# Optimization experiments

Hardware: AMD Instinct MI355X
Metric: run time of the kernel (lower is better)

The kernel has to match this reference:

```python
import jax, jax.numpy as jnp
import numpy as np

D_HEAD = 64
EPS_NORM = 1e-6
EPS_COS = 1e-6


def rms_norm(x, scale, eps=EPS_NORM):
    mean_sq = jnp.mean(x * x, axis=-1, keepdims=True)
    return x * (scale * jax.lax.rsqrt(mean_sq + eps))


def setup_inputs() -> dict:
    key = jax.random.key(0)
    ks = jax.random.split(key, 8)
    b, l, d, d_ff = 2, 2048, 1024, 3072
    std = 1.0 / np.sqrt(d)
    return {
        "x": jax.random.normal(ks[0], (b, l, d), jnp.float32),
        "pos": jax.random.normal(ks[1], (b, l, 2), jnp.float32),
        "norm_scale": jnp.ones((d,), jnp.float32),
        "w_qkv": jax.random.normal(ks[2], (3 * d, d), jnp.float32) * std,
        "attn_scale": jnp.full((d // D_HEAD,), 10.0, jnp.float32),
        "w_out": jax.random.normal(ks[3], (d, d), jnp.float32) * std,
        "ff_norm_scale": jnp.ones((d,), jnp.float32),
        "w_up": jax.random.normal(ks[4], (2 * d_ff, d), jnp.float32) * std,
        "w_down": jax.random.normal(ks[5], (d, d_ff), jnp.float32) * (1.0 / np.sqrt(d_ff)),
    }


def reference(x, pos, norm_scale, w_qkv, attn_scale, w_out, ff_norm_scale, w_up, w_down):
    n, l, d = x.shape
    nh = d // D_HEAD

    # ---- self-attention block ----
    skip = x
    xn = rms_norm(x, norm_scale)
    qkv = xn @ w_qkv.T                                    # [n, l, 3d]
    qkv = qkv.reshape(n, l, 3, nh, D_HEAD).transpose(2, 0, 3, 1, 4)  # [3, n, nh, l, e]
    q, k, v = qkv[0], qkv[1], qkv[2]

    # cosine-similarity rescaling with per-head learned scale
    s = attn_scale[:, None, None]                         # [nh, 1, 1]
    sqrt_s = jnp.sqrt(s)
    q = q * (sqrt_s * jax.lax.rsqrt(jnp.sum(q * q, axis=-1, keepdims=True) + EPS_COS))
    k = k * (sqrt_s * jax.lax.rsqrt(jnp.sum(k * k, axis=-1, keepdims=True) + EPS_COS))

    # SDPA with scale=1.0 (no RoPE: rope_cls=None)
    scores = jnp.einsum("nhqe,nhke->nhqk", q, k)
    attn = jax.nn.softmax(scores, axis=-1)
    o = jnp.einsum("nhqk,nhke->nhqe", attn, v)            # [n, nh, l, e]
    o = o.transpose(0, 2, 1, 3).reshape(n, l, d)
    x = o @ w_out.T + skip

    # ---- feed-forward block (SwiGLU) ----
    skip = x
    xn = rms_norm(x, ff_norm_scale)
    u = xn @ w_up.T                                       # [n, l, 2*d_ff]
    a, g = jnp.split(u, 2, axis=-1)
    h = a * jax.nn.silu(g)
    x = h @ w_down.T + skip
    return x
```

## Files before the change

kernel.cpp:

```cpp
#include <hip/hip_runtime.h>
#include <cstdint>
#include <cstddef>
#include <cstdio>


typedef unsigned short u16;
typedef __bf16 bf16x8 __attribute__((ext_vector_type(8)));
typedef float  f32x4  __attribute__((ext_vector_type(4)));

__device__ __forceinline__ u16 f2b(float f) {
  return __builtin_bit_cast(u16, (__bf16)f);
}
__device__ __forceinline__ float b2f(u16 u) {
  return (float)__builtin_bit_cast(__bf16, u);
}

__device__ __forceinline__ void cp16(const u16* g, u16* l) {
  __builtin_amdgcn_global_load_lds(
      (__attribute__((address_space(1))) void*)(uintptr_t)g,
      (__attribute__((address_space(3))) void*)(uintptr_t)l,
      16, 0, 0);
}

template <int MODE>
__global__ __launch_bounds__(256) void gemm_bt(
    const u16* __restrict__ A, const u16* __restrict__ B,
    float* __restrict__ Cf, u16* __restrict__ Cb, const float* __restrict__ res,
    int M, int N, int K, int lda)
{
  __shared__ __align__(16) u16 lsA[128 * 64];
  __shared__ __align__(16) u16 lsB[128 * 64];
  const int t = threadIdx.x;
  const int w = t >> 6, lane = t & 63;
  const int wm = (w >> 1) * 64, wn = (w & 1) * 64;
  const int lr = lane & 15, quad = lane >> 4;
  const int cswz = lr & 7;
  const size_t rowA0 = (size_t)blockIdx.x * 128;
  const size_t rowB0 = (size_t)blockIdx.y * 128;

  f32x4 acc[4][4] = {};

  for (int k0 = 0; k0 < K; k0 += 64) {
#pragma unroll
    for (int i = 0; i < 4; ++i) {
      const int id = i * 256 + t;
      const int r = id >> 3;
      const int c = ((id & 7) ^ (r & 7)) * 8;
      cp16(A + (rowA0 + r) * lda + k0 + c, lsA + id * 8);
      cp16(B + (rowB0 + r) * (size_t)K + k0 + c, lsB + id * 8);
    }
    __syncthreads();
#pragma unroll
    for (int ks = 0; ks < 2; ++ks) {
      const int co = ((ks * 4 + quad) ^ cswz) * 8;
      bf16x8 af[4], bfr[4];
#pragma unroll
      for (int i = 0; i < 4; ++i) {
        af[i]  = *(const bf16x8*)(lsA + (wm + i * 16 + lr) * 64 + co);
        bfr[i] = *(const bf16x8*)(lsB + (wn + i * 16 + lr) * 64 + co);
      }
#pragma unroll
      for (int mi = 0; mi < 4; ++mi)
#pragma unroll
        for (int ni = 0; ni < 4; ++ni)
          acc[mi][ni] = __builtin_amdgcn_mfma_f32_16x16x32_bf16(
              af[mi], bfr[ni], acc[mi][ni], 0, 0, 0);
    }
    __syncthreads();
  }

#pragma unroll
  for (int mi = 0; mi < 4; ++mi) {
#pragma unroll
    for (int r = 0; r < 4; ++r) {
      const size_t m = rowA0 + wm + mi * 16 + quad * 4 + r;
#pragma unroll
      for (int ni = 0; ni < 4; ++ni) {
        const size_t n = rowB0 + wn + ni * 16 + lr;
        const size_t o = m * (size_t)N + n;
        const float v = acc[mi][ni][r];
        if (MODE == 0) Cf[o] = v;
        else if (MODE == 1) Cf[o] = v + res[o];
        else Cb[o] = f2b(v);
      }
    }
  }
}

__global__ __launch_bounds__(256) void rmsnorm_k(
    const float* __restrict__ x, const float* __restrict__ g, u16* __restrict__ out)
{
  const int row = blockIdx.x;
  const int t = threadIdx.x;
  const float4 a = ((const float4*)(x + (size_t)row * 1024))[t];
  float ss = a.x * a.x + a.y * a.y + a.z * a.z + a.w * a.w;
#pragma unroll
  for (int o = 32; o; o >>= 1) ss += __shfl_xor(ss, o, 64);
  __shared__ float red[4];
  if ((t & 63) == 0) red[t >> 6] = ss;
  __syncthreads();
  ss = red[0] + red[1] + red[2] + red[3];
  const float r = rsqrtf(ss * (1.0f / 1024.0f) + 1e-6f);
  const float4 gg = ((const float4*)g)[t];
  ushort4 o4;
  o4.x = f2b(a.x * gg.x * r);
  o4.y = f2b(a.y * gg.y * r);
  o4.z = f2b(a.z * gg.z * r);
  o4.w = f2b(a.w * gg.w * r);
  ((ushort4*)out)[(size_t)row * 256 + t] = o4;
}

__global__ __launch_bounds__(256) void cvt_bf16_k(
    const float* __restrict__ in, u16* __restrict__ out)
{
  const size_t i = (size_t)blockIdx.x * 256 + threadIdx.x;
  const float4 v = ((const float4*)in)[i];
  ushort4 o4;
  o4.x = f2b(v.x); o4.y = f2b(v.y); o4.z = f2b(v.z); o4.w = f2b(v.w);
  ((ushort4*)out)[i] = o4;
}

__global__ __launch_bounds__(256) void qkv_prep_k(
    const u16* __restrict__ qkv, const float* __restrict__ attn_scale,
    u16* __restrict__ Qb, u16* __restrict__ Kb, u16* __restrict__ Vt)
{
  const int l0 = blockIdx.x * 64;
  const int h  = blockIdx.y;
  const int nb = blockIdx.z;
  const int t = threadIdx.x, w = t >> 6, lane = t & 63;
  __shared__ float lsV[64][65];
  const float sq = sqrtf(attn_scale[h]);
  const int head = nb * 16 + h;
#pragma unroll 4
  for (int i = 0; i < 16; ++i) {
    const int lrow = i * 4 + w;
    const int l = l0 + lrow;
    const u16* base = qkv + ((size_t)nb * 2048 + l) * 3072 + h * 64 + lane;
    const float qv = b2f(base[0]);
    const float kv = b2f(base[1024]);
    const float vv = b2f(base[2048]);
    float ssq = qv * qv, ssk = kv * kv;
#pragma unroll
    for (int o = 32; o; o >>= 1) {
      ssq += __shfl_xor(ssq, o, 64);
      ssk += __shfl_xor(ssk, o, 64);
    }
    const size_t gb = ((size_t)head * 2048 + l) * 64 + lane;
    Qb[gb] = f2b(qv * sq * rsqrtf(ssq + 1e-6f));
    Kb[gb] = f2b(kv * sq * rsqrtf(ssk + 1e-6f));
    lsV[lrow][lane] = vv;
  }
  __syncthreads();
  const int e = t >> 2, p = t & 3;
  union { u16 s[16]; uint4 v[2]; } tmp;
#pragma unroll
  for (int j = 0; j < 16; ++j) tmp.s[j] = f2b(lsV[p * 16 + j][e]);
  u16* dst = Vt + ((size_t)head * 64 + e) * 2048 + l0 + p * 16;
  *(uint4*)dst = tmp.v[0];
  *(uint4*)(dst + 8) = tmp.v[1];
}

__global__ __launch_bounds__(256) void attn_k(
    const u16* __restrict__ Qb, const u16* __restrict__ Kb,
    const u16* __restrict__ Vt, u16* __restrict__ O)
{
  const int l0 = blockIdx.x * 64;
  const int head = blockIdx.y;
  const int nb = head >> 4, h = head & 15;
  const int t = threadIdx.x, w = t >> 6, lane = t & 63;
  const int lr = lane & 15, quad = lane >> 4;
  const int cswz = lr & 7;
  __shared__ __align__(16) u16 lsK[2][64 * 64];
  __shared__ __align__(16) u16 lsV[2][64 * 64];
  __shared__ __align__(16) u16 lsP[4][16 * 64];
  u16* myP = lsP[w];
  const size_t hb = (size_t)head << 17;

  const int sr = t >> 3;
  const int sc = ((t & 7) ^ (sr & 7)) * 8;
  const u16* Kg = Kb + hb + (size_t)sr * 64 + sc;
  const u16* Vg = Vt + hb + (size_t)sr * 2048 + sc;

  const int qrow = l0 + w * 16 + lr;
  const u16* qp = Qb + hb + (size_t)qrow * 64;
  const bf16x8 qf0 = *(const bf16x8*)(qp + quad * 8);
  const bf16x8 qf1 = *(const bf16x8*)(qp + 32 + quad * 8);

  f32x4 oacc[4] = {};
  float rsv[4] = {0.f, 0.f, 0.f, 0.f};

  cp16(Kg, lsK[0] + t * 8);
  cp16(Kg + 32 * 64, lsK[0] + 32 * 64 + t * 8);
  cp16(Vg, lsV[0] + t * 8);
  cp16(Vg + 32 * 2048, lsV[0] + 32 * 64 + t * 8);

  int cur = 0;
  for (int k0 = 0; k0 < 2048; k0 += 64) {
    __syncthreads();
    if (k0 + 64 < 2048) {
      const int nxt = cur ^ 1;
      const u16* Kn = Kg + (size_t)(k0 + 64) * 64;
      const u16* Vn = Vg + (k0 + 64);
      cp16(Kn, lsK[nxt] + t * 8);
      cp16(Kn + 32 * 64, lsK[nxt] + 32 * 64 + t * 8);
      cp16(Vn, lsV[nxt] + t * 8);
      cp16(Vn + 32 * 2048, lsV[nxt] + 32 * 64 + t * 8);
    }
    const u16* kb = lsK[cur];
    const u16* vb = lsV[cur];

#pragma unroll
    for (int ni = 0; ni < 4; ++ni) {
      const int krow = (ni * 16 + lr) * 64;
      const bf16x8 b0 = *(const bf16x8*)(kb + krow + ((quad ^ cswz) * 8));
      const bf16x8 b1 = *(const bf16x8*)(kb + krow + (((4 + quad) ^ cswz) * 8));
      f32x4 s = {};
      s = __builtin_amdgcn_mfma_f32_16x16x32_bf16(qf0, b0, s, 0, 0, 0);
      s = __builtin_amdgcn_mfma_f32_16x16x32_bf16(qf1, b1, s, 0, 0, 0);
      const int pchunk = ni * 2 + (lr >> 3);
#pragma unroll
      for (int r = 0; r < 4; ++r) {
        const float p = __expf(s[r]);
        rsv[r] += p;
        const int prow = quad * 4 + r;
        myP[prow * 64 + ((pchunk ^ (prow & 7)) << 3) + (lane & 7)] = f2b(p);
      }
    }
    asm volatile("" ::: "memory");
#pragma unroll
    for (int ks = 0; ks < 2; ++ks) {
      const bf16x8 af = *(const bf16x8*)(myP + lr * 64 + (((ks * 4 + quad) ^ cswz) << 3));
#pragma unroll
      for (int ei = 0; ei < 4; ++ei) {
        const bf16x8 bv = *(const bf16x8*)(vb + (ei * 16 + lr) * 64 + (((ks * 4 + quad) ^ cswz) << 3));
        oacc[ei] = __builtin_amdgcn_mfma_f32_16x16x32_bf16(af, bv, oacc[ei], 0, 0, 0);
      }
    }
    asm volatile("" ::: "memory");
    cur ^= 1;
  }

#pragma unroll
  for (int r = 0; r < 4; ++r) {
    float v = rsv[r];
    v += __shfl_xor(v, 1, 64);
    v += __shfl_xor(v, 2, 64);
    v += __shfl_xor(v, 4, 64);
    v += __shfl_xor(v, 8, 64);
    rsv[r] = 1.0f / v;
  }
#pragma unroll
  for (int r = 0; r < 4; ++r) {
    const int l = l0 + w * 16 + quad * 4 + r;
    u16* ob = O + ((size_t)nb * 2048 + l) * 1024 + h * 64;
#pragma unroll
    for (int ei = 0; ei < 4; ++ei)
      ob[ei * 16 + lr] = f2b(oacc[ei][r] * rsv[r]);
  }
}

__global__ __launch_bounds__(256) void swiglu_k(u16* __restrict__ u)
{
  const unsigned j = ((unsigned)blockIdx.x * 256 + threadIdx.x) * 8;
  const unsigned row = j / 3072u, col = j % 3072u;
  u16* ap = u + (size_t)row * 6144 + col;
  union { u16 s[8]; uint4 v; } a, g, hh;
  a.v = *(const uint4*)ap;
  g.v = *(const uint4*)(ap + 3072);
#pragma unroll
  for (int i = 0; i < 8; ++i) {
    const float av = b2f(a.s[i]);
    const float gv = b2f(g.s[i]);
    hh.s[i] = f2b(av * (gv / (1.0f + __expf(-gv))));
  }
  *(uint4*)ap = hh.v;
}

static constexpr size_t WQKV_B = 0;
static constexpr size_t WOUT_B = WQKV_B + 6291456;
static constexpr size_t WUP_B  = WOUT_B + 2097152;
static constexpr size_t WDN_B  = WUP_B + 12582912;
static constexpr size_t XN_B   = WDN_B + 6291456;
static constexpr size_t Q_B    = XN_B + 8388608;
static constexpr size_t K_B    = Q_B + 8388608;
static constexpr size_t VT_B   = K_B + 8388608;
static constexpr size_t O_B    = VT_B + 8388608;
static constexpr size_t BIG_B  = O_B + 8388608;
static constexpr size_t WS_NEED = BIG_B + 50331648;

extern "C" void kernel_launch(void* const* d_in, const int* in_sizes, int n_in,
                              void* d_out, int out_size, void* d_ws, size_t ws_size,
                              hipStream_t stream)
{
  (void)in_sizes; (void)n_in; (void)out_size;
  if (ws_size < WS_NEED) {
    fprintf(stderr, "kernel_launch: ws_size %zu < required %zu\n", ws_size, WS_NEED);
    return;
  }
  const float* x          = (const float*)d_in[0];
  const float* norm_scale = (const float*)d_in[2];
  const float* w_qkv      = (const float*)d_in[3];
  const float* attn_scale = (const float*)d_in[4];
  const float* w_out      = (const float*)d_in[5];
  const float* ff_scale   = (const float*)d_in[6];
  const float* w_up       = (const float*)d_in[7];
  const float* w_down     = (const float*)d_in[8];
  float* out = (float*)d_out;
  char* ws = (char*)d_ws;

  u16* wqkv_b = (u16*)(ws + WQKV_B);
  u16* wout_b = (u16*)(ws + WOUT_B);
  u16* wup_b  = (u16*)(ws + WUP_B);
  u16* wdn_b  = (u16*)(ws + WDN_B);
  u16* xn     = (u16*)(ws + XN_B);
  u16* Qb     = (u16*)(ws + Q_B);
  u16* Kb     = (u16*)(ws + K_B);
  u16* Vtb    = (u16*)(ws + VT_B);
  u16* Ob     = (u16*)(ws + O_B);
  u16* qkvb   = (u16*)(ws + BIG_B);
  u16* ub     = (u16*)(ws + BIG_B);

  cvt_bf16_k<<<3072, 256, 0, stream>>>(w_qkv, wqkv_b);
  cvt_bf16_k<<<1024, 256, 0, stream>>>(w_out, wout_b);
  cvt_bf16_k<<<6144, 256, 0, stream>>>(w_up,  wup_b);
  cvt_bf16_k<<<3072, 256, 0, stream>>>(w_down, wdn_b);

  rmsnorm_k<<<4096, 256, 0, stream>>>(x, norm_scale, xn);
  gemm_bt<2><<<dim3(32, 24), 256, 0, stream>>>(xn, wqkv_b, nullptr, qkvb, nullptr,
                                               4096, 3072, 1024, 1024);
  qkv_prep_k<<<dim3(32, 16, 2), 256, 0, stream>>>(qkvb, attn_scale, Qb, Kb, Vtb);
  attn_k<<<dim3(32, 32), 256, 0, stream>>>(Qb, Kb, Vtb, Ob);
  gemm_bt<1><<<dim3(32, 8), 256, 0, stream>>>(Ob, wout_b, out, nullptr, x,
                                              4096, 1024, 1024, 1024);
  rmsnorm_k<<<4096, 256, 0, stream>>>(out, ff_scale, xn);
  gemm_bt<2><<<dim3(32, 48), 256, 0, stream>>>(xn, wup_b, nullptr, ub, nullptr,
                                               4096, 6144, 1024, 1024);
  swiglu_k<<<6144, 256, 0, stream>>>(ub);
  gemm_bt<1><<<dim3(32, 8), 256, 0, stream>>>(ub, wdn_b, out, nullptr, out,
                                              4096, 1024, 3072, 6144);
}
```

Measured before the change: 386.3 us.

## Switch attention to 32x32x16 MFMA with 128 query rows per block

The attention kernel now gives each wave 32 query rows instead of 16 and uses 32x32x16 bf16 MFMA for both QK^T and PV. Each block covers 128 queries, which halves the grid and doubles how often each K/V tile staged in LDS is reused. The P staging layout, the swizzles and the row-sum reduction (one extra shuffle) are rewritten to match the 32x32 accumulator layout. In exchange the kernel uses more registers per thread and launches only 512 blocks, which may reduce occupancy.

```diff
diff --git a/kernel.cpp b/kernel.cpp
--- a/kernel.cpp
+++ b/kernel.cpp
@@ -7,6 +7,7 @@
 typedef unsigned short u16;
 typedef __bf16 bf16x8 __attribute__((ext_vector_type(8)));
 typedef float  f32x4  __attribute__((ext_vector_type(4)));
+typedef float  f32x16 __attribute__((ext_vector_type(16)));
 
 __device__ __forceinline__ u16 f2b(float f) {
   return __builtin_bit_cast(u16, (__bf16)f);
@@ -164,15 +165,14 @@
     const u16* __restrict__ Qb, const u16* __restrict__ Kb,
     const u16* __restrict__ Vt, u16* __restrict__ O)
 {
-  const int l0 = blockIdx.x * 64;
+  const int l0 = blockIdx.x * 128;
   const int head = blockIdx.y;
   const int nb = head >> 4, h = head & 15;
   const int t = threadIdx.x, w = t >> 6, lane = t & 63;
-  const int lr = lane & 15, quad = lane >> 4;
-  const int cswz = lr & 7;
+  const int lm = lane & 31, h2 = lane >> 5;
   __shared__ __align__(16) u16 lsK[2][64 * 64];
   __shared__ __align__(16) u16 lsV[2][64 * 64];
-  __shared__ __align__(16) u16 lsP[4][16 * 64];
+  __shared__ __align__(16) u16 lsP[4][32 * 64];
   u16* myP = lsP[w];
   const size_t hb = (size_t)head << 17;
 
@@ -181,13 +181,16 @@
   const u16* Kg = Kb + hb + (size_t)sr * 64 + sc;
   const u16* Vg = Vt + hb + (size_t)sr * 2048 + sc;
 
-  const int qrow = l0 + w * 16 + lr;
-  const u16* qp = Qb + hb + (size_t)qrow * 64;
-  const bf16x8 qf0 = *(const bf16x8*)(qp + quad * 8);
-  const bf16x8 qf1 = *(const bf16x8*)(qp + 32 + quad * 8);
-
-  f32x4 oacc[4] = {};
-  float rsv[4] = {0.f, 0.f, 0.f, 0.f};
+  const int qrow = l0 + w * 32 + lm;
+  const u16* qp = Qb + hb + (size_t)qrow * 64 + h2 * 8;
+  bf16x8 qf[4];
+#pragma unroll
+  for (int c = 0; c < 4; ++c) qf[c] = *(const bf16x8*)(qp + c * 16);
+
+  f32x16 oacc[2] = {};
+  float rsv[16];
+#pragma unroll
+  for (int r = 0; r < 16; ++r) rsv[r] = 0.f;
 
   cp16(Kg, lsK[0] + t * 8);
   cp16(Kg + 32 * 64, lsK[0] + 32 * 64 + t * 8);
@@ -210,30 +213,33 @@
     const u16* vb = lsV[cur];
 
 #pragma unroll
-    for (int ni = 0; ni < 4; ++ni) {
-      const int krow = (ni * 16 + lr) * 64;
-      const bf16x8 b0 = *(const bf16x8*)(kb + krow + ((quad ^ cswz) * 8));
-      const bf16x8 b1 = *(const bf16x8*)(kb + krow + (((4 + quad) ^ cswz) * 8));
-      f32x4 s = {};
-      s = __builtin_amdgcn_mfma_f32_16x16x32_bf16(qf0, b0, s, 0, 0, 0);
-      s = __builtin_amdgcn_mfma_f32_16x16x32_bf16(qf1, b1, s, 0, 0, 0);
-      const int pchunk = ni * 2 + (lr >> 3);
-#pragma unroll
-      for (int r = 0; r < 4; ++r) {
+    for (int ni = 0; ni < 2; ++ni) {
+      const int krow = ni * 32 + lm;
+      const int kswz = krow & 7;
+      f32x16 s = {};
+#pragma unroll
+      for (int c = 0; c < 4; ++c) {
+        const bf16x8 bk = *(const bf16x8*)(kb + krow * 64 + (((c * 2 + h2) ^ kswz) << 3));
+        s = __builtin_amdgcn_mfma_f32_32x32x16_bf16(qf[c], bk, s, 0, 0, 0);
+      }
+      const int pc = ni * 4 + (lm >> 3);
+#pragma unroll
+      for (int r = 0; r < 16; ++r) {
         const float p = __expf(s[r]);
         rsv[r] += p;
-        const int prow = quad * 4 + r;
-        myP[prow * 64 + ((pchunk ^ (prow & 7)) << 3) + (lane & 7)] = f2b(p);
+        const int q2 = (r & 3) + 8 * (r >> 2) + 4 * h2;
+        myP[q2 * 64 + ((pc ^ (q2 & 7)) << 3) + (lm & 7)] = f2b(p);
       }
     }
     asm volatile("" ::: "memory");
 #pragma unroll
-    for (int ks = 0; ks < 2; ++ks) {
-      const bf16x8 af = *(const bf16x8*)(myP + lr * 64 + (((ks * 4 + quad) ^ cswz) << 3));
-#pragma unroll
-      for (int ei = 0; ei < 4; ++ei) {
-        const bf16x8 bv = *(const bf16x8*)(vb + (ei * 16 + lr) * 64 + (((ks * 4 + quad) ^ cswz) << 3));
-        oacc[ei] = __builtin_amdgcn_mfma_f32_16x16x32_bf16(af, bv, oacc[ei], 0, 0, 0);
+    for (int kc = 0; kc < 4; ++kc) {
+      const bf16x8 ap = *(const bf16x8*)(myP + lm * 64 + (((kc * 2 + h2) ^ (lm & 7)) << 3));
+#pragma unroll
+      for (int ei = 0; ei < 2; ++ei) {
+        const int vrow = ei * 32 + lm;
+        const bf16x8 bv = *(const bf16x8*)(vb + vrow * 64 + (((kc * 2 + h2) ^ (vrow & 7)) << 3));
+        oacc[ei] = __builtin_amdgcn_mfma_f32_32x32x16_bf16(ap, bv, oacc[ei], 0, 0, 0);
       }
     }
     asm volatile("" ::: "memory");
@@ -241,21 +247,23 @@
   }
 
 #pragma unroll
-  for (int r = 0; r < 4; ++r) {
+  for (int r = 0; r < 16; ++r) {
     float v = rsv[r];
     v += __shfl_xor(v, 1, 64);
     v += __shfl_xor(v, 2, 64);
     v += __shfl_xor(v, 4, 64);
     v += __shfl_xor(v, 8, 64);
+    v += __shfl_xor(v, 16, 64);
     rsv[r] = 1.0f / v;
   }
 #pragma unroll
-  for (int r = 0; r < 4; ++r) {
-    const int l = l0 + w * 16 + quad * 4 + r;
+  for (int r = 0; r < 16; ++r) {
+    const int q2 = (r & 3) + 8 * (r >> 2) + 4 * h2;
+    const int l = l0 + w * 32 + q2;
     u16* ob = O + ((size_t)nb * 2048 + l) * 1024 + h * 64;
 #pragma unroll
-    for (int ei = 0; ei < 4; ++ei)
-      ob[ei * 16 + lr] = f2b(oacc[ei][r] * rsv[r]);
+    for (int ei = 0; ei < 2; ++ei)
+      ob[ei * 32 + lm] = f2b(oacc[ei][r] * rsv[r]);
   }
 }
 
@@ -329,7 +337,7 @@
   gemm_bt<2><<<dim3(32, 24), 256, 0, stream>>>(xn, wqkv_b, nullptr, qkvb, nullptr,
                                                4096, 3072, 1024, 1024);
   qkv_prep_k<<<dim3(32, 16, 2), 256, 0, stream>>>(qkvb, attn_scale, Qb, Kb, Vtb);
-  attn_k<<<dim3(32, 32), 256, 0, stream>>>(Qb, Kb, Vtb, Ob);
+  attn_k<<<dim3(16, 32), 256, 0, stream>>>(Qb, Kb, Vtb, Ob);
   gemm_bt<1><<<dim3(32, 8), 256, 0, stream>>>(Ob, wout_b, out, nullptr, x,
                                               4096, 1024, 1024, 1024);
   rmsnorm_k<<<4096, 256, 0, stream>>>(out, ff_scale, xn);
```

Measured after the change: 391.5 us. Within noise of the previous version (+1.3%).

## Keep attention probabilities in registers via transposed MFMA; narrow N-tiles for output GEMMs

Applied to the files above, without the earlier changes.

The attention kernel now computes scores transposed (K as the A operand, Q as B), so each lane's exp'd probabilities already match the B-operand layout of a 16x16x16 bf16 MFMA against V. This removes the per-wave LDS staging buffer for P, its writes, reads and memory barriers, at the cost of more, smaller MFMAs and 8-byte V reads from LDS. Separately, the GEMM gains a BN template parameter, and the two N=1024 GEMMs use BN=64 to double the block count from 256 to 512, improving CU occupancy at the cost of less B-tile reuse per block.

```diff
diff --git a/kernel.cpp b/kernel.cpp
--- a/kernel.cpp
+++ b/kernel.cpp
@@ -6,6 +6,7 @@
 
 typedef unsigned short u16;
 typedef __bf16 bf16x8 __attribute__((ext_vector_type(8)));
+typedef short  s16x4  __attribute__((ext_vector_type(4)));
 typedef float  f32x4  __attribute__((ext_vector_type(4)));
 
 __device__ __forceinline__ u16 f2b(float f) {
@@ -22,23 +23,24 @@
       16, 0, 0);
 }
 
-template <int MODE>
+template <int MODE, int BN>
 __global__ __launch_bounds__(256) void gemm_bt(
     const u16* __restrict__ A, const u16* __restrict__ B,
     float* __restrict__ Cf, u16* __restrict__ Cb, const float* __restrict__ res,
     int M, int N, int K, int lda)
 {
+  constexpr int NI = BN / 32;
   __shared__ __align__(16) u16 lsA[128 * 64];
-  __shared__ __align__(16) u16 lsB[128 * 64];
+  __shared__ __align__(16) u16 lsB[BN * 64];
   const int t = threadIdx.x;
   const int w = t >> 6, lane = t & 63;
-  const int wm = (w >> 1) * 64, wn = (w & 1) * 64;
+  const int wm = (w >> 1) * 64, wn = (w & 1) * (BN / 2);
   const int lr = lane & 15, quad = lane >> 4;
   const int cswz = lr & 7;
   const size_t rowA0 = (size_t)blockIdx.x * 128;
-  const size_t rowB0 = (size_t)blockIdx.y * 128;
-
-  f32x4 acc[4][4] = {};
+  const size_t rowB0 = (size_t)blockIdx.y * BN;
+
+  f32x4 acc[4][NI] = {};
 
   for (int k0 = 0; k0 < K; k0 += 64) {
 #pragma unroll
@@ -47,22 +49,29 @@
       const int r = id >> 3;
       const int c = ((id & 7) ^ (r & 7)) * 8;
       cp16(A + (rowA0 + r) * lda + k0 + c, lsA + id * 8);
+    }
+#pragma unroll
+    for (int i = 0; i < BN / 32; ++i) {
+      const int id = i * 256 + t;
+      const int r = id >> 3;
+      const int c = ((id & 7) ^ (r & 7)) * 8;
       cp16(B + (rowB0 + r) * (size_t)K + k0 + c, lsB + id * 8);
     }
     __syncthreads();
 #pragma unroll
     for (int ks = 0; ks < 2; ++ks) {
       const int co = ((ks * 4 + quad) ^ cswz) * 8;
-      bf16x8 af[4], bfr[4];
-#pragma unroll
-      for (int i = 0; i < 4; ++i) {
-        af[i]  = *(const bf16x8*)(lsA + (wm + i * 16 + lr) * 64 + co);
+      bf16x8 af[4], bfr[NI];
+#pragma unroll
+      for (int i = 0; i < 4; ++i)
+        af[i] = *(const bf16x8*)(lsA + (wm + i * 16 + lr) * 64 + co);
+#pragma unroll
+      for (int i = 0; i < NI; ++i)
         bfr[i] = *(const bf16x8*)(lsB + (wn + i * 16 + lr) * 64 + co);
-      }
 #pragma unroll
       for (int mi = 0; mi < 4; ++mi)
 #pragma unroll
-        for (int ni = 0; ni < 4; ++ni)
+        for (int ni = 0; ni < NI; ++ni)
           acc[mi][ni] = __builtin_amdgcn_mfma_f32_16x16x32_bf16(
               af[mi], bfr[ni], acc[mi][ni], 0, 0, 0);
     }
@@ -75,7 +84,7 @@
     for (int r = 0; r < 4; ++r) {
       const size_t m = rowA0 + wm + mi * 16 + quad * 4 + r;
 #pragma unroll
-      for (int ni = 0; ni < 4; ++ni) {
+      for (int ni = 0; ni < NI; ++ni) {
         const size_t n = rowB0 + wn + ni * 16 + lr;
         const size_t o = m * (size_t)N + n;
         const float v = acc[mi][ni][r];
@@ -169,11 +178,8 @@
   const int nb = head >> 4, h = head & 15;
   const int t = threadIdx.x, w = t >> 6, lane = t & 63;
   const int lr = lane & 15, quad = lane >> 4;
-  const int cswz = lr & 7;
   __shared__ __align__(16) u16 lsK[2][64 * 64];
   __shared__ __align__(16) u16 lsV[2][64 * 64];
-  __shared__ __align__(16) u16 lsP[4][16 * 64];
-  u16* myP = lsP[w];
   const size_t hb = (size_t)head << 17;
 
   const int sr = t >> 3;
@@ -182,12 +188,12 @@
   const u16* Vg = Vt + hb + (size_t)sr * 2048 + sc;
 
   const int qrow = l0 + w * 16 + lr;
-  const u16* qp = Qb + hb + (size_t)qrow * 64;
-  const bf16x8 qf0 = *(const bf16x8*)(qp + quad * 8);
-  const bf16x8 qf1 = *(const bf16x8*)(qp + 32 + quad * 8);
-
-  f32x4 oacc[4] = {};
-  float rsv[4] = {0.f, 0.f, 0.f, 0.f};
+  const u16* qp = Qb + hb + (size_t)qrow * 64 + quad * 8;
+  const bf16x8 qf0 = *(const bf16x8*)qp;
+  const bf16x8 qf1 = *(const bf16x8*)(qp + 32);
+
+  f32x4 ot[4] = {};
+  float rs = 0.f;
 
   cp16(Kg, lsK[0] + t * 8);
   cp16(Kg + 32 * 64, lsK[0] + 32 * 64 + t * 8);
@@ -210,52 +216,46 @@
     const u16* vb = lsV[cur];
 
 #pragma unroll
-    for (int ni = 0; ni < 4; ++ni) {
-      const int krow = (ni * 16 + lr) * 64;
-      const bf16x8 b0 = *(const bf16x8*)(kb + krow + ((quad ^ cswz) * 8));
-      const bf16x8 b1 = *(const bf16x8*)(kb + krow + (((4 + quad) ^ cswz) * 8));
+    for (int kt = 0; kt < 4; ++kt) {
+      const int krow = (kt * 16 + lr) * 64;
+      const int kswz = lr & 7;
+      const bf16x8 a0 = *(const bf16x8*)(kb + krow + ((quad ^ kswz) << 3));
+      const bf16x8 a1 = *(const bf16x8*)(kb + krow + (((4 + quad) ^ kswz) << 3));
       f32x4 s = {};
-      s = __builtin_amdgcn_mfma_f32_16x16x32_bf16(qf0, b0, s, 0, 0, 0);
-      s = __builtin_amdgcn_mfma_f32_16x16x32_bf16(qf1, b1, s, 0, 0, 0);
-      const int pchunk = ni * 2 + (lr >> 3);
+      s = __builtin_amdgcn_mfma_f32_16x16x32_bf16(a0, qf0, s, 0, 0, 0);
+      s = __builtin_amdgcn_mfma_f32_16x16x32_bf16(a1, qf1, s, 0, 0, 0);
+      s16x4 pf;
 #pragma unroll
       for (int r = 0; r < 4; ++r) {
         const float p = __expf(s[r]);
-        rsv[r] += p;
-        const int prow = quad * 4 + r;
-        myP[prow * 64 + ((pchunk ^ (prow & 7)) << 3) + (lane & 7)] = f2b(p);
+        rs += p;
+        pf[r] = (short)f2b(p);
       }
-    }
-    asm volatile("" ::: "memory");
-#pragma unroll
-    for (int ks = 0; ks < 2; ++ks) {
-      const bf16x8 af = *(const bf16x8*)(myP + lr * 64 + (((ks * 4 + quad) ^ cswz) << 3));
+      const int vc = kt * 2 + (quad >> 1);
+      const int vh = (quad & 1) * 4;
 #pragma unroll
       for (int ei = 0; ei < 4; ++ei) {
-        const bf16x8 bv = *(const bf16x8*)(vb + (ei * 16 + lr) * 64 + (((ks * 4 + quad) ^ cswz) << 3));
-        oacc[ei] = __builtin_amdgcn_mfma_f32_16x16x32_bf16(af, bv, oacc[ei], 0, 0, 0);
+        const int vrow = ei * 16 + lr;
+        const s16x4 vf = *(const s16x4*)(vb + vrow * 64 + ((vc ^ (vrow & 7)) << 3) + vh);
+        ot[ei] = __builtin_amdgcn_mfma_f32_16x16x16bf16_1k(vf, pf, ot[ei], 0, 0, 0);
       }
     }
-    asm volatile("" ::: "memory");
     cur ^= 1;
   }
 
-#pragma unroll
-  for (int r = 0; r < 4; ++r) {
-    float v = rsv[r];
-    v += __shfl_xor(v, 1, 64);
-    v += __shfl_xor(v, 2, 64);
-    v += __shfl_xor(v, 4, 64);
-    v += __shfl_xor(v, 8, 64);
-    rsv[r] = 1.0f / v;
-  }
-#pragma unroll
-  for (int r = 0; r < 4; ++r) {
-    const int l = l0 + w * 16 + quad * 4 + r;
-    u16* ob = O + ((size_t)nb * 2048 + l) * 1024 + h * 64;
-#pragma unroll
-    for (int ei = 0; ei < 4; ++ei)
-      ob[ei * 16 + lr] = f2b(oacc[ei][r] * rsv[r]);
+  rs += __shfl_xor(rs, 16, 64);
+  rs += __shfl_xor(rs, 32, 64);
+  const float inv = 1.0f / rs;
+
+  u16* ob = O + ((size_t)nb * 2048 + l0 + w * 16 + lr) * 1024 + h * 64 + quad * 4;
+#pragma unroll
+  for (int ei = 0; ei < 4; ++ei) {
+    ushort4 o4;
+    o4.x = f2b(ot[ei][0] * inv);
+    o4.y = f2b(ot[ei][1] * inv);
+    o4.z = f2b(ot[ei][2] * inv);
+    o4.w = f2b(ot[ei][3] * inv);
+    *(ushort4*)(ob + ei * 16) = o4;
   }
 }
 
@@ -326,16 +326,16 @@
   cvt_bf16_k<<<3072, 256, 0, stream>>>(w_down, wdn_b);
 
   rmsnorm_k<<<4096, 256, 0, stream>>>(x, norm_scale, xn);
-  gemm_bt<2><<<dim3(32, 24), 256, 0, stream>>>(xn, wqkv_b, nullptr, qkvb, nullptr,
-                                               4096, 3072, 1024, 1024);
+  gemm_bt<2, 128><<<dim3(32, 24), 256, 0, stream>>>(xn, wqkv_b, nullptr, qkvb,
+                                                    nullptr, 4096, 3072, 1024, 1024);
   qkv_prep_k<<<dim3(32, 16, 2), 256, 0, stream>>>(qkvb, attn_scale, Qb, Kb, Vtb);
   attn_k<<<dim3(32, 32), 256, 0, stream>>>(Qb, Kb, Vtb, Ob);
-  gemm_bt<1><<<dim3(32, 8), 256, 0, stream>>>(Ob, wout_b, out, nullptr, x,
-                                              4096, 1024, 1024, 1024);
+  gemm_bt<1, 64><<<dim3(32, 16), 256, 0, stream>>>(Ob, wout_b, out, nullptr, x,
+                                                   4096, 1024, 1024, 1024);
   rmsnorm_k<<<4096, 256, 0, stream>>>(out, ff_scale, xn);
-  gemm_bt<2><<<dim3(32, 48), 256, 0, stream>>>(xn, wup_b, nullptr, ub, nullptr,
-                                               4096, 6144, 1024, 1024);
+  gemm_bt<2, 128><<<dim3(32, 48), 256, 0, stream>>>(xn, wup_b, nullptr, ub, nullptr,
+                                                    4096, 6144, 1024, 1024);
   swiglu_k<<<6144, 256, 0, stream>>>(ub);
-  gemm_bt<1><<<dim3(32, 8), 256, 0, stream>>>(ub, wdn_b, out, nullptr, out,
-                                              4096, 1024, 3072, 6144);
-}
+  gemm_bt<1, 64><<<dim3(32, 16), 256, 0, stream>>>(ub, wdn_b, out, nullptr, out,
+                                                   4096, 1024, 3072, 6144);
+}
```

New measurement: 368.5 us. 1.05x faster.
